# Kernel tuning notes

Measured on AMD Instinct MI355X. Metric: run time of the kernel, lower is better.

## Reference

```python
import jax, jax.numpy as jnp
import numpy as np

N, E = 50000, 800000
IN_C, EDGE_IN, HID, HEADS = 16, 16, 32, 4


def setup_inputs() -> dict:
    key = jax.random.key(0)
    ks = jax.random.split(key, 16)
    HC = HEADS * HID
    def lin(k, fan_in, shape):
        b = 1.0 / np.sqrt(fan_in)
        return jax.random.uniform(k, shape, jnp.float32, -b, b)
    return {
        "x": jax.random.normal(ks[0], (N, IN_C), jnp.float32),
        "edge_index": jax.random.randint(ks[1], (2, E), 0, N, jnp.int64),
        "edge_attr": jax.random.normal(ks[2], (E, EDGE_IN), jnp.float32),
        # TransformerConv params
        "Wq": lin(ks[3], IN_C, (IN_C, HC)), "bq": lin(ks[4], IN_C, (HC,)),
        "Wk": lin(ks[5], IN_C, (IN_C, HC)), "bk": lin(ks[6], IN_C, (HC,)),
        "Wv": lin(ks[7], IN_C, (IN_C, HC)), "bv": lin(ks[8], IN_C, (HC,)),
        "We": lin(ks[9], EDGE_IN, (EDGE_IN, HC)),  # lin_edge has no bias in PyG
        "Wskip": lin(ks[10], IN_C, (IN_C, HID)), "bskip": lin(ks[11], IN_C, (HID,)),
        # edge MLP params
        "W1": lin(ks[12], 2 * HID + EDGE_IN, (2 * HID + EDGE_IN, HID)),
        "b1": lin(ks[13], 2 * HID + EDGE_IN, (HID,)),
        "W2": lin(ks[14], HID, (HID, 1)), "b2": lin(ks[15], HID, (1,)),
    }


def _forward(x, edge_attr, Wq, bq, Wk, bk, Wv, bv, We, Wskip, bskip, W1, b1, W2, b2, src, dst):
    n = x.shape[0]
    q = (x @ Wq + bq).reshape(n, HEADS, HID)
    k = (x @ Wk + bk).reshape(n, HEADS, HID)
    v = (x @ Wv + bv).reshape(n, HEADS, HID)
    e = (edge_attr @ We).reshape(-1, HEADS, HID)  # [E,H,C]
    kj = k[src] + e                               # key of source node + edge emb
    alpha = jnp.einsum('ehc,ehc->eh', q[dst], kj) / jnp.sqrt(jnp.float32(HID))
    # segment softmax over incoming edges of each dst node (per head)
    m = jax.ops.segment_max(alpha, dst, num_segments=n)      # [N,H]
    a = jnp.exp(alpha - m[dst])
    s = jax.ops.segment_sum(a, dst, num_segments=n)          # [N,H]
    a = a / s[dst]
    msg = (v[src] + e) * a[:, :, None]                        # [E,H,C]
    out = jax.ops.segment_sum(msg, dst, num_segments=n)      # [N,H,C]
    out = out.mean(axis=1)                                    # concat=False -> mean over heads
    out = out + x @ Wskip + bskip                              # root/skip connection
    # edge MLP on gather-concat features
    feat = jnp.concatenate([out[src], edge_attr, out[dst]], axis=-1)
    h = jax.nn.relu(feat @ W1 + b1)
    return (h @ W2 + b2).reshape(-1)


def reference(x, edge_index, edge_attr, Wq, bq, Wk, bk, Wv, bv, We, Wskip, bskip, W1, b1, W2, b2):
    src, dst = edge_index[0], edge_index[1]
    return _forward(x, edge_attr, Wq, bq, Wk, bk, Wv, bv, We, Wskip, bskip, W1, b1, W2, b2, src, dst)
```

## Files before the change

### kernel.cpp

```cpp
#include <hip/hip_runtime.h>
#include <hip/hip_fp16.h>

#define NN 50000
#define NE 800000
#define NB 196
#define EPB 3125
#define NODE_BLOCKS 12500

#define SL 0.25506413f

#define PMV 0
#define MEV 1024
#define BEV 2048
#define UPV 2112
#define WPV 2176
#define WCV 2240
#define P_TOTAL 2304

template <int CTRL>
__device__ __forceinline__ float dpp_add(float v) {
  int m = __builtin_amdgcn_update_dpp(0, __builtin_bit_cast(int, v), CTRL, 0xF, 0xF, true);
  return v + __builtin_bit_cast(float, m);
}
__device__ __forceinline__ float row16_reduce(float v) {
  v = dpp_add<0xB1>(v);
  v = dpp_add<0x4E>(v);
  v = dpp_add<0x124>(v);
  v = dpp_add<0x128>(v);
  return v;
}

__global__ __launch_bounds__(256) void precompute_kernel(
    const float* __restrict__ Wq, const float* __restrict__ Wk,
    const float* __restrict__ bq, const float* __restrict__ bk,
    const float* __restrict__ We, float* __restrict__ P) {
  int t = threadIdx.x;
  for (int idx = t; idx < 1024; idx += 256) {
    int lane = idx >> 4, i = idx & 15;
    int h = lane >> 4, tt = lane & 15;
    float am = 0.f, ae = 0.f;
#pragma unroll
    for (int c = 0; c < 32; c++) {
      float wq = Wq[i * 128 + h * 32 + c];
      am += wq * Wk[tt * 128 + h * 32 + c];
      ae += wq * We[tt * 128 + h * 32 + c];
    }
    P[PMV + idx] = am * SL;
    P[MEV + idx] = ae * SL;
  }
  if (t < 64) {
    int h = t >> 4, tt = t & 15;
    float be = 0.f, up = 0.f, wp = 0.f;
#pragma unroll
    for (int c = 0; c < 32; c++) {
      be += bq[h * 32 + c] * We[tt * 128 + h * 32 + c];
      up += Wq[tt * 128 + h * 32 + c] * bk[h * 32 + c];
      wp += bq[h * 32 + c] * Wk[tt * 128 + h * 32 + c];
    }
    P[BEV + t] = be * SL;
    P[UPV + t] = up * SL;
    P[WPV + t] = wp * SL;
  }
  if (t < 4) {
    float wc = 0.f;
#pragma unroll
    for (int c = 0; c < 32; c++) wc += bq[t * 32 + c] * bk[t * 32 + c];
    P[WCV + t] = wc * SL;
  }
}

__global__ __launch_bounds__(256) void node_linear_kernel(
    const float* __restrict__ x, const float* __restrict__ P,
    const int* __restrict__ ei, int* __restrict__ hist_all,
    float* __restrict__ y, float* __restrict__ qe,
    float* __restrict__ u4, float* __restrict__ w4) {
  __shared__ int hist[NB];
  if (blockIdx.x >= NODE_BLOCKS) {
    int b = blockIdx.x - NODE_BLOCKS;
    int t = threadIdx.x;
    if (t < NB) hist[t] = 0;
    __syncthreads();
    int base = b * EPB;
    for (int i = t; i < EPB; i += 256)
      atomicAdd(&hist[ei[NE + base + i] >> 8], 1);
    __syncthreads();
    if (t < NB) hist_all[t * 256 + b] = hist[t];
    return;
  }
  int wave = threadIdx.x >> 6;
  int lane = threadIdx.x & 63;
  int n = blockIdx.x * 4 + wave;
  int h = lane >> 4, t = lane & 15;

  const float4* xp = (const float4*)(x + n * 16);
  float4 X0 = xp[0], X1 = xp[1], X2 = xp[2], X3 = xp[3];
  float xr[16] = {X0.x, X0.y, X0.z, X0.w, X1.x, X1.y, X1.z, X1.w,
                  X2.x, X2.y, X2.z, X2.w, X3.x, X3.y, X3.z, X3.w};

  const float4* pm = (const float4*)(P + PMV) + lane * 4;
  const float4* me = (const float4*)(P + MEV) + lane * 4;
  float yt = 0.f, qv = P[BEV + lane];
#pragma unroll
  for (int i4 = 0; i4 < 4; i4++) {
    float4 m = pm[i4], e = me[i4];
    yt += xr[4 * i4] * m.x + xr[4 * i4 + 1] * m.y
        + xr[4 * i4 + 2] * m.z + xr[4 * i4 + 3] * m.w;
    qv += xr[4 * i4] * e.x + xr[4 * i4 + 1] * e.y
        + xr[4 * i4 + 2] * e.z + xr[4 * i4 + 3] * e.w;
  }
  y[n * 64 + lane] = yt;
  qe[n * 64 + lane] = qv;

  float pu = P[UPV + lane] * xr[t];
  float pw = P[WPV + lane] * xr[t];
  pu = row16_reduce(pu);
  pw = row16_reduce(pw);
  if (t == 0) {
    u4[n * 4 + h] = pu;
    w4[n * 4 + h] = pw + P[WCV + h];
  }
}

__global__ __launch_bounds__(256) void scan_buckets_kernel(
    int* __restrict__ hist_all, int* __restrict__ btot) {
  int wv = blockIdx.x * 4 + (threadIdx.x >> 6);
  int l = threadIdx.x & 63;
  if (wv >= NB) return;
  int base = wv * 256;
  int run = 0;
#pragma unroll
  for (int c = 0; c < 4; c++) {
    int v = hist_all[base + c * 64 + l];
    int orig = v;
#pragma unroll
    for (int d = 1; d < 64; d <<= 1) {
      int u = __shfl_up(v, d);
      if (l >= d) v += u;
    }
    hist_all[base + c * 64 + l] = run + v - orig;
    run += __shfl(v, 63);
  }
  if (l == 0) btot[wv] = run;
}

__global__ __launch_bounds__(256) void tiny_scan_kernel(
    const int* __restrict__ btot, int* __restrict__ coarse_offs) {
  __shared__ int sc[256];
  int t = threadIdx.x;
  int v = (t < NB) ? btot[t] : 0;
  sc[t] = v;
  __syncthreads();
  for (int d = 1; d < 256; d <<= 1) {
    int u = (t >= d) ? sc[t - d] : 0;
    __syncthreads();
    sc[t] += u;
    __syncthreads();
  }
  if (t < NB) coarse_offs[t] = sc[t] - v;
  if (t == NB - 1) coarse_offs[NB] = sc[t];
}

__global__ __launch_bounds__(256) void bucket_scatter_kernel(
    const int* __restrict__ ei, const float* __restrict__ edge_attr,
    const int* __restrict__ cursor_all, const int* __restrict__ coarse_offs,
    int2* __restrict__ s_tmp, uint4* __restrict__ ea_tmp) {
  __shared__ int cur[NB];
  int t = threadIdx.x, b = blockIdx.x;
  if (t < NB) cur[t] = cursor_all[t * 256 + b] + coarse_offs[t];
  __syncthreads();
  int base = b * EPB;
  for (int i = t; i < EPB; i += 256) {
    int e = base + i;
    int src = ei[e], dst = ei[NE + e];
    const float4* eap = (const float4*)(edge_attr + (size_t)e * 16);
    float4 a = eap[0], bb = eap[1], c = eap[2], d = eap[3];
    uint4 u0, u1;
    __half2 hh;
    hh = __floats2half2_rn(a.x, a.y);   u0.x = *(unsigned*)&hh;
    hh = __floats2half2_rn(a.z, a.w);   u0.y = *(unsigned*)&hh;
    hh = __floats2half2_rn(bb.x, bb.y); u0.z = *(unsigned*)&hh;
    hh = __floats2half2_rn(bb.z, bb.w); u0.w = *(unsigned*)&hh;
    hh = __floats2half2_rn(c.x, c.y);   u1.x = *(unsigned*)&hh;
    hh = __floats2half2_rn(c.z, c.w);   u1.y = *(unsigned*)&hh;
    hh = __floats2half2_rn(d.x, d.y);   u1.z = *(unsigned*)&hh;
    hh = __floats2half2_rn(d.z, d.w);   u1.w = *(unsigned*)&hh;
    int pos = atomicAdd(&cur[dst >> 8], 1);
    s_tmp[pos] = make_int2(src | ((dst & 255) << 16), e);
    ea_tmp[(size_t)pos * 2]     = u0;
    ea_tmp[(size_t)pos * 2 + 1] = u1;
  }
}

__global__ __launch_bounds__(256) void fine_csr_kernel(
    const int2* __restrict__ s_tmp, const uint4* __restrict__ ea_tmp,
    const int* __restrict__ coarse_offs,
    int2* __restrict__ s_se, uint4* __restrict__ s_ea4,
    int* __restrict__ offs) {
  __shared__ int cnt[256], sc[256], cur[256];
  int t = threadIdx.x, b = blockIdx.x;
  int lo = coarse_offs[b], hi = coarse_offs[b + 1];
  cnt[t] = 0;
  __syncthreads();
  for (int p = lo + t; p < hi; p += 256)
    atomicAdd(&cnt[(s_tmp[p].x >> 16) & 255], 1);
  __syncthreads();
  int myc = cnt[t];
  sc[t] = myc;
  __syncthreads();
  for (int d = 1; d < 256; d <<= 1) {
    int v = (t >= d) ? sc[t - d] : 0;
    __syncthreads();
    sc[t] += v;
    __syncthreads();
  }
  int excl = sc[t] - myc;
  cur[t] = lo + excl;
  int gd = b * 256 + t;
  if (gd <= NN) offs[gd] = lo + excl;
  __syncthreads();
  for (int p = lo + t; p < hi; p += 256) {
    int2 m = s_tmp[p];
    uint4 u0 = ea_tmp[(size_t)p * 2];
    uint4 u1 = ea_tmp[(size_t)p * 2 + 1];
    int pos = atomicAdd(&cur[(m.x >> 16) & 255], 1);
    s_se[pos] = make_int2(m.x & 0xFFFF, m.y);
    s_ea4[(size_t)pos * 2]     = u0;
    s_ea4[(size_t)pos * 2 + 1] = u1;
  }
}

__global__ __launch_bounds__(256) void aggregate_kernel(
    const float* __restrict__ y, const float* __restrict__ qe,
    const float* __restrict__ u4, const float* __restrict__ w4,
    const float* __restrict__ x, const __half* __restrict__ s_ea,
    const int2* __restrict__ s_se,
    const float* __restrict__ We, const float* __restrict__ Wv,
    const float* __restrict__ bv,
    const float* __restrict__ Wskip, const float* __restrict__ bskip,
    const float* __restrict__ W1, const float* __restrict__ b1,
    const int* __restrict__ offs,
    __half* __restrict__ Ah, __half* __restrict__ Cbh) {
  int wave = threadIdx.x >> 6, lane = threadIdx.x & 63;
  int n = blockIdx.x * 4 + wave;
  int h = lane >> 4, t = lane & 15;
  int base = h * 32 + t;
  int gb = lane & 48;

  float yt = y[n * 64 + lane];
  float qet = qe[n * 64 + lane];
  float u_n = u4[n * 4 + h];
  int off = offs[n], end = offs[n + 1];

  float s = 0.f, ax = 0.f, ae = 0.f;
  int j = off;
  for (; j + 8 <= end; j += 8) {
    const uint4* sp = (const uint4*)&s_se[j];
    uint4 sa = sp[0], sb = sp[1], sc4 = sp[2], sd = sp[3];
    int src[8] = {(int)sa.x, (int)sa.z, (int)sb.x, (int)sb.z,
                  (int)sc4.x, (int)sc4.z, (int)sd.x, (int)sd.z};
    float xs[8], ea[8], uw[8];
#pragma unroll
    for (int u = 0; u < 8; u++) {
      xs[u] = x[(unsigned)src[u] * 16u + (unsigned)t];
      ea[u] = __half2float(s_ea[(size_t)(j + u) * 16 + t]);
      uw[u] = w4[(unsigned)src[u] * 4u + (unsigned)h];
    }
    float p[8];
#pragma unroll
    for (int u = 0; u < 8; u++) p[u] = fmaf(yt, xs[u], qet * ea[u]);
#pragma unroll
    for (int u = 0; u < 8; u++) p[u] = row16_reduce(p[u]);
#pragma unroll
    for (int u = 0; u < 8; u++) {
      float wgt = exp2f(p[u] + u_n + uw[u]);
      s += wgt;
      ax = fmaf(wgt, xs[u], ax);
      ae = fmaf(wgt, ea[u], ae);
    }
  }
  for (; j < end; j++) {
    int srcu = s_se[j].x;
    float xs = x[(unsigned)srcu * 16u + (unsigned)t];
    float ea_ = __half2float(s_ea[(size_t)j * 16 + t]);
    float uw = w4[(unsigned)srcu * 4u + (unsigned)h];
    float p = fmaf(yt, xs, qet * ea_);
    p = row16_reduce(p);
    float wgt = exp2f(p + u_n + uw);
    s += wgt;
    ax = fmaf(wgt, xs, ax);
    ae = fmaf(wgt, ea_, ae);
  }

  float inv = (end > off) ? 1.f / s : 0.f;
  float dflag = (end > off) ? 1.f : 0.f;
  float axn = ax * inv, aen = ae * inv;
  float r0 = dflag * bv[base], r1 = dflag * bv[base + 16];
#pragma unroll
  for (int i = 0; i < 16; i++) {
    float axi = __shfl(axn, gb | i);
    float aei = __shfl(aen, gb | i);
    r0 += axi * Wv[i * 128 + base]      + aei * We[i * 128 + base];
    r1 += axi * Wv[i * 128 + base + 16] + aei * We[i * 128 + base + 16];
  }
  r0 += __shfl_xor(r0, 16); r0 += __shfl_xor(r0, 32);
  r1 += __shfl_xor(r1, 16); r1 += __shfl_xor(r1, 32);

  float sk0 = bskip[t], sk1 = bskip[t + 16];
#pragma unroll
  for (int i = 0; i < 16; i++) {
    float xi = x[n * 16 + i];
    sk0 += xi * Wskip[i * 32 + t];
    sk1 += xi * Wskip[i * 32 + t + 16];
  }
  float o0 = 0.25f * r0 + sk0;
  float o1 = 0.25f * r1 + sk1;

  int jj = lane & 31;
  int roff = (lane < 32) ? 0 : 48;
  float acc = (lane < 32) ? 0.f : b1[jj];
#pragma unroll
  for (int i = 0; i < 16; i++) {
    float oi = __shfl(o0, i);
    acc += oi * W1[(roff + i) * 32 + jj];
  }
#pragma unroll
  for (int i = 0; i < 16; i++) {
    float oi = __shfl(o1, i);
    acc += oi * W1[(roff + 16 + i) * 32 + jj];
  }
  float nb = __shfl_xor(acc, 1);
  if ((lane & 1) == 0) {
    __half2 hh = __floats2half2_rn(acc, nb);
    if (lane < 32) *(__half2*)(Ah  + n * 32 + jj) = hh;
    else           *(__half2*)(Cbh + n * 32 + jj) = hh;
  }
}

__global__ __launch_bounds__(256) void mlp_kernel(
    const int2* __restrict__ s_se, const __half* __restrict__ s_ea,
    const int* __restrict__ offs,
    const __half* __restrict__ Ah, const __half* __restrict__ Cbh,
    const float* __restrict__ W1, const float* __restrict__ W2,
    const float* __restrict__ b2v, float* __restrict__ out) {
  int wave = threadIdx.x >> 6, lane = threadIdx.x & 63;
  int n = blockIdx.x * 4 + wave;
  int g = lane >> 5, l = lane & 31;

  float w1e[16];
#pragma unroll
  for (int i = 0; i < 16; i++) w1e[i] = W1[(32 + i) * 32 + l];
  float w2j = W2[l];
  float b2s = b2v[0];
  float cb = __half2float(Cbh[n * 32 + l]);
  int off = offs[n], end = offs[n + 1];

  for (int p = off + g; p < end; p += 2) {
    int2 se = s_se[p];
    float a = __half2float(Ah[(unsigned)se.x * 32u + l]);
    const uint4* eap = (const uint4*)(s_ea + (size_t)p * 16);
    uint4 u0 = eap[0], u1 = eap[1];
    float hsum = a + cb;
    const __half2* hp0 = (const __half2*)&u0;
    const __half2* hp1 = (const __half2*)&u1;
#pragma unroll
    for (int i = 0; i < 4; i++) {
      float2 f0 = __half22float2(hp0[i]);
      hsum += f0.x * w1e[2 * i] + f0.y * w1e[2 * i + 1];
      float2 f1 = __half22float2(hp1[i]);
      hsum += f1.x * w1e[8 + 2 * i] + f1.y * w1e[8 + 2 * i + 1];
    }
    float hv = fmaxf(hsum, 0.f) * w2j;
    hv += __shfl_xor(hv, 1); hv += __shfl_xor(hv, 2);
    hv += __shfl_xor(hv, 4); hv += __shfl_xor(hv, 8);
    hv += __shfl_xor(hv, 16);
    if (l == 0) out[se.y] = hv + b2s;
  }
}

extern "C" void kernel_launch(void* const* d_in, const int* in_sizes, int n_in,
                              void* d_out, int out_size, void* d_ws, size_t ws_size,
                              hipStream_t stream) {
  const float* x         = (const float*)d_in[0];
  const int*   ei        = (const int*)d_in[1];
  const float* edge_attr = (const float*)d_in[2];
  const float* Wq = (const float*)d_in[3],  *bq = (const float*)d_in[4];
  const float* Wk = (const float*)d_in[5],  *bk = (const float*)d_in[6];
  const float* Wv = (const float*)d_in[7],  *bv = (const float*)d_in[8];
  const float* We = (const float*)d_in[9];
  const float* Wskip = (const float*)d_in[10], *bskip = (const float*)d_in[11];
  const float* W1 = (const float*)d_in[12], *b1 = (const float*)d_in[13];
  const float* W2 = (const float*)d_in[14], *b2 = (const float*)d_in[15];
  float* out = (float*)d_out;

  char* w = (char*)d_ws;
  float*   y    = (float*)w;            w += (size_t)NN * 64 * 4;
  float*   qe   = (float*)w;            w += (size_t)NN * 64 * 4;
  float*   u4   = (float*)w;            w += (size_t)NN * 4 * 4;
  float*   w4   = (float*)w;            w += (size_t)NN * 4 * 4;
  int2*    s_se = (int2*)w;             w += (size_t)NE * 8;
  int2*    s_tmp = (int2*)w;            w += (size_t)NE * 8;
  uint4*   s_ea4 = (uint4*)w;           w += (size_t)NE * 32;
  uint4*   ea_tmp = (uint4*)w;
  __half*  Ah   = (__half*)ea_tmp;
  __half*  Cbh  = (__half*)((char*)ea_tmp + (size_t)NN * 32 * 2);
  w += (size_t)NE * 32;
  int*     hist_all = (int*)w;          w += (size_t)256 * 256 * 4;
  int*     btot = (int*)w;              w += 256 * 4;
  int*     coarse_offs = (int*)w;       w += 256 * 4;
  int*     offs = (int*)w;              w += ((size_t)NN + 1) * 4;
  float*   P    = (float*)w;            w += (size_t)P_TOTAL * 4;

  precompute_kernel<<<1, 256, 0, stream>>>(Wq, Wk, bq, bk, We, P);
  node_linear_kernel<<<NODE_BLOCKS + 256, 256, 0, stream>>>(
      x, P, ei, hist_all, y, qe, u4, w4);
  scan_buckets_kernel<<<49, 256, 0, stream>>>(hist_all, btot);
  tiny_scan_kernel<<<1, 256, 0, stream>>>(btot, coarse_offs);
  bucket_scatter_kernel<<<256, 256, 0, stream>>>(ei, edge_attr, hist_all,
                                                 coarse_offs, s_tmp, ea_tmp);
  fine_csr_kernel<<<NB, 256, 0, stream>>>(s_tmp, ea_tmp, coarse_offs,
                                          s_se, s_ea4, offs);
  aggregate_kernel<<<NN / 4, 256, 0, stream>>>(y, qe, u4, w4, x,
                                               (const __half*)s_ea4, s_se,
                                               We, Wv, bv, Wskip, bskip, W1, b1,
                                               offs, Ah, Cbh);
  mlp_kernel<<<NN / 4, 256, 0, stream>>>(s_se, (const __half*)s_ea4, offs,
                                         Ah, Cbh, W1, W2, b2, out);
}
```

Baseline: 259.5 us.

## Place fp16 edge attributes once via CSR position map instead of two-stage move

Edge attributes are no longer converted and moved through the intermediate bucket buffer and then the fine CSR pass. The fine CSR kernel now records each edge's final CSR position, and a new kernel reads edge_attr, converts it to half and scatters it straight to that slot. This removes one 32-byte-per-edge write and read of the temporary buffer, at the cost of an extra launch, a 4-byte position array and scattered 32-byte writes. It also switches the MLP reduction to the DPP row16 reduce and moves the Ah/Cbh scratch into the s_tmp region.

```diff
diff --git a/kernel.cpp b/kernel.cpp
--- a/kernel.cpp
+++ b/kernel.cpp
@@ -161,9 +161,8 @@
 }
 
 __global__ __launch_bounds__(256) void bucket_scatter_kernel(
-    const int* __restrict__ ei, const float* __restrict__ edge_attr,
-    const int* __restrict__ cursor_all, const int* __restrict__ coarse_offs,
-    int2* __restrict__ s_tmp, uint4* __restrict__ ea_tmp) {
+    const int* __restrict__ ei, const int* __restrict__ cursor_all,
+    const int* __restrict__ coarse_offs, int2* __restrict__ s_tmp) {
   __shared__ int cur[NB];
   int t = threadIdx.x, b = blockIdx.x;
   if (t < NB) cur[t] = cursor_all[t * 256 + b] + coarse_offs[t];
@@ -172,29 +171,14 @@
   for (int i = t; i < EPB; i += 256) {
     int e = base + i;
     int src = ei[e], dst = ei[NE + e];
-    const float4* eap = (const float4*)(edge_attr + (size_t)e * 16);
-    float4 a = eap[0], bb = eap[1], c = eap[2], d = eap[3];
-    uint4 u0, u1;
-    __half2 hh;
-    hh = __floats2half2_rn(a.x, a.y);   u0.x = *(unsigned*)&hh;
-    hh = __floats2half2_rn(a.z, a.w);   u0.y = *(unsigned*)&hh;
-    hh = __floats2half2_rn(bb.x, bb.y); u0.z = *(unsigned*)&hh;
-    hh = __floats2half2_rn(bb.z, bb.w); u0.w = *(unsigned*)&hh;
-    hh = __floats2half2_rn(c.x, c.y);   u1.x = *(unsigned*)&hh;
-    hh = __floats2half2_rn(c.z, c.w);   u1.y = *(unsigned*)&hh;
-    hh = __floats2half2_rn(d.x, d.y);   u1.z = *(unsigned*)&hh;
-    hh = __floats2half2_rn(d.z, d.w);   u1.w = *(unsigned*)&hh;
     int pos = atomicAdd(&cur[dst >> 8], 1);
     s_tmp[pos] = make_int2(src | ((dst & 255) << 16), e);
-    ea_tmp[(size_t)pos * 2]     = u0;
-    ea_tmp[(size_t)pos * 2 + 1] = u1;
   }
 }
 
 __global__ __launch_bounds__(256) void fine_csr_kernel(
-    const int2* __restrict__ s_tmp, const uint4* __restrict__ ea_tmp,
-    const int* __restrict__ coarse_offs,
-    int2* __restrict__ s_se, uint4* __restrict__ s_ea4,
+    const int2* __restrict__ s_tmp, const int* __restrict__ coarse_offs,
+    int2* __restrict__ s_se, int* __restrict__ csrpos,
     int* __restrict__ offs) {
   __shared__ int cnt[256], sc[256], cur[256];
   int t = threadIdx.x, b = blockIdx.x;
@@ -220,13 +204,31 @@
   __syncthreads();
   for (int p = lo + t; p < hi; p += 256) {
     int2 m = s_tmp[p];
-    uint4 u0 = ea_tmp[(size_t)p * 2];
-    uint4 u1 = ea_tmp[(size_t)p * 2 + 1];
     int pos = atomicAdd(&cur[(m.x >> 16) & 255], 1);
     s_se[pos] = make_int2(m.x & 0xFFFF, m.y);
-    s_ea4[(size_t)pos * 2]     = u0;
-    s_ea4[(size_t)pos * 2 + 1] = u1;
-  }
+    csrpos[m.y] = pos;
+  }
+}
+
+__global__ __launch_bounds__(256) void ea_place_kernel(
+    const float* __restrict__ edge_attr, const int* __restrict__ csrpos,
+    uint4* __restrict__ s_ea4) {
+  int e = blockIdx.x * 256 + threadIdx.x;
+  const float4* eap = (const float4*)(edge_attr + (size_t)e * 16);
+  float4 a = eap[0], bb = eap[1], c = eap[2], d = eap[3];
+  uint4 u0, u1;
+  __half2 hh;
+  hh = __floats2half2_rn(a.x, a.y);   u0.x = *(unsigned*)&hh;
+  hh = __floats2half2_rn(a.z, a.w);   u0.y = *(unsigned*)&hh;
+  hh = __floats2half2_rn(bb.x, bb.y); u0.z = *(unsigned*)&hh;
+  hh = __floats2half2_rn(bb.z, bb.w); u0.w = *(unsigned*)&hh;
+  hh = __floats2half2_rn(c.x, c.y);   u1.x = *(unsigned*)&hh;
+  hh = __floats2half2_rn(c.z, c.w);   u1.y = *(unsigned*)&hh;
+  hh = __floats2half2_rn(d.x, d.y);   u1.z = *(unsigned*)&hh;
+  hh = __floats2half2_rn(d.z, d.w);   u1.w = *(unsigned*)&hh;
+  int pos = csrpos[e];
+  s_ea4[(size_t)pos * 2]     = u0;
+  s_ea4[(size_t)pos * 2 + 1] = u1;
 }
 
 __global__ __launch_bounds__(256) void aggregate_kernel(
@@ -370,8 +372,7 @@
       hsum += f1.x * w1e[8 + 2 * i] + f1.y * w1e[8 + 2 * i + 1];
     }
     float hv = fmaxf(hsum, 0.f) * w2j;
-    hv += __shfl_xor(hv, 1); hv += __shfl_xor(hv, 2);
-    hv += __shfl_xor(hv, 4); hv += __shfl_xor(hv, 8);
+    hv = row16_reduce(hv);
     hv += __shfl_xor(hv, 16);
     if (l == 0) out[se.y] = hv + b2s;
   }
@@ -398,12 +399,12 @@
   float*   u4   = (float*)w;            w += (size_t)NN * 4 * 4;
   float*   w4   = (float*)w;            w += (size_t)NN * 4 * 4;
   int2*    s_se = (int2*)w;             w += (size_t)NE * 8;
-  int2*    s_tmp = (int2*)w;            w += (size_t)NE * 8;
+  int2*    s_tmp = (int2*)w;
+  __half*  Ah   = (__half*)s_tmp;
+  __half*  Cbh  = (__half*)((char*)s_tmp + (size_t)NN * 32 * 2);
+  w += (size_t)NE * 8;
   uint4*   s_ea4 = (uint4*)w;           w += (size_t)NE * 32;
-  uint4*   ea_tmp = (uint4*)w;
-  __half*  Ah   = (__half*)ea_tmp;
-  __half*  Cbh  = (__half*)((char*)ea_tmp + (size_t)NN * 32 * 2);
-  w += (size_t)NE * 32;
+  int*     csrpos = (int*)w;            w += (size_t)NE * 4;
   int*     hist_all = (int*)w;          w += (size_t)256 * 256 * 4;
   int*     btot = (int*)w;              w += 256 * 4;
   int*     coarse_offs = (int*)w;       w += 256 * 4;
@@ -415,10 +416,11 @@
       x, P, ei, hist_all, y, qe, u4, w4);
   scan_buckets_kernel<<<49, 256, 0, stream>>>(hist_all, btot);
   tiny_scan_kernel<<<1, 256, 0, stream>>>(btot, coarse_offs);
-  bucket_scatter_kernel<<<256, 256, 0, stream>>>(ei, edge_attr, hist_all,
-                                                 coarse_offs, s_tmp, ea_tmp);
-  fine_csr_kernel<<<NB, 256, 0, stream>>>(s_tmp, ea_tmp, coarse_offs,
-                                          s_se, s_ea4, offs);
+  bucket_scatter_kernel<<<256, 256, 0, stream>>>(ei, hist_all, coarse_offs,
+                                                 s_tmp);
+  fine_csr_kernel<<<NB, 256, 0, stream>>>(s_tmp, coarse_offs, s_se, csrpos,
+                                          offs);
+  ea_place_kernel<<<NE / 256, 256, 0, stream>>>(edge_attr, csrpos, s_ea4);
   aggregate_kernel<<<NN / 4, 256, 0, stream>>>(y, qe, u4, w4, x,
                                                (const __half*)s_ea4, s_se,
                                                We, Wv, bv, Wskip, bskip, W1, b1,
```

New measurement: 253.9 us. 1.02x faster.
